# Optimization experiments

Measured on AMD Instinct MI355X. Metric: run time of the kernel, lower is better.

## Reference

```python
import jax, jax.numpy as jnp
import numpy as np

# DkNetCL (ConformalLayers): depth x [Conv2d(3x3, pad=1, no bias) + SRePro], then Linear(32768 -> 10).
# ConformalLayers algebraically fuses the cascade in conformal space; the equivalent Euclidean math
# per layer is: x <- conv(x); x <- x * 2*alpha^2 / (2*alpha^2 + ||x||^2), where ||x|| is the l2 norm
# of the ENTIRE flattened feature map of each sample (the sample is a single point in conformal space).
# alpha fixed to 1.0 (cl.SRePro() default is weight-adaptive; a constant keeps the reference deterministic).

DEPTH = 4
ALPHA = 1.0


def _conv(x, w):
    # x: [B, Cin, H, W], w: [Cout, Cin, 3, 3], stride 1, padding 1 (shape-preserving)
    return jax.lax.conv_general_dilated(
        x, w, window_strides=(1, 1), padding=((1, 1), (1, 1)),
        dimension_numbers=("NCHW", "OIHW", "NCHW"))


def _srepro(x, alpha):
    # per-sample squared norm over the whole feature map
    sq = jnp.sum(x * x, axis=(1, 2, 3), keepdims=True)  # [B,1,1,1]
    two_a2 = 2.0 * alpha * alpha
    return x * (two_a2 / (two_a2 + sq))


def setup_inputs() -> dict:
    key = jax.random.key(0)
    ks = jax.random.split(key, DEPTH + 2)
    B, H, W = 1024, 32, 32
    x = jax.random.normal(ks[0], (B, 3, H, W), jnp.float32)
    inp = {"x": x}
    cin = 3
    for i in range(DEPTH):
        fan_in = cin * 9
        inp[f"conv_w{i}"] = jax.random.normal(ks[1 + i], (32, cin, 3, 3), jnp.float32) / np.sqrt(fan_in).astype(np.float32)
        cin = 32
    flat = 32 * H * W  # 32768
    inp["fc_w"] = jax.random.normal(ks[-1], (10, flat), jnp.float32) / np.sqrt(flat).astype(np.float32)
    inp["fc_b"] = jnp.zeros((10,), jnp.float32)
    return inp


def reference(x, conv_w0, conv_w1, conv_w2, conv_w3, fc_w, fc_b):
    for w in (conv_w0, conv_w1, conv_w2, conv_w3):
        x = _srepro(_conv(x, w), ALPHA)
    x = x.reshape(x.shape[0], -1)  # [B, 32768]
    return x @ fc_w.T + fc_b  # [B, 10]
```

## Files before the change

### kernel.cpp

```cpp
#include <hip/hip_runtime.h>
#include <stdint.h>


typedef __bf16 bf16x8 __attribute__((ext_vector_type(8)));
typedef float f32x4 __attribute__((ext_vector_type(4)));
typedef unsigned short u16;
typedef unsigned int u32;

__device__ __forceinline__ u16 f2bf(float f) {
    union { float f; u32 i; } v; v.f = f;
    u32 r = v.i + 0x7FFFu + ((v.i >> 16) & 1u);
    return (u16)(r >> 16);
}
__device__ __forceinline__ float bf2f(u16 u) {
    union { u32 i; float f; } v; v.i = ((u32)u) << 16;
    return v.f;
}
union frag_cast { uint4 u; bf16x8 f; };

__global__ void prep_weights_k(const float* __restrict__ w0, const float* __restrict__ w1,
                               const float* __restrict__ w2, const float* __restrict__ w3,
                               u16* __restrict__ wfrag)
{
    int idx = blockIdx.x * 256 + threadIdx.x;
    if (idx >= 4 * 9 * 2 * 64) return;
    int lane  = idx & 63;
    int mh    = (idx >> 6) & 1;
    int tap   = (idx >> 7) % 9;
    int layer = (idx >> 7) / 9;
    const float* w = layer == 0 ? w0 : layer == 1 ? w1 : layer == 2 ? w2 : w3;
    int cin_act = (layer == 0) ? 3 : 32;
    int cout = mh * 16 + (lane & 15);
    int cin0 = (lane >> 4) * 8;
    int dy = tap / 3, dx = tap % 3;
    u16 v[8];
    for (int j = 0; j < 8; j++) {
        int cin = cin0 + j;
        float f = (cin < cin_act) ? w[((cout * cin_act + cin) * 3 + dy) * 3 + dx] : 0.f;
        v[j] = f2bf(f);
    }
    uint4 pack;
    pack.x = (u32)v[0] | ((u32)v[1] << 16);
    pack.y = (u32)v[2] | ((u32)v[3] << 16);
    pack.z = (u32)v[4] | ((u32)v[5] << 16);
    pack.w = (u32)v[6] | ((u32)v[7] << 16);
    reinterpret_cast<uint4*>(wfrag)[idx] = pack;
}

__global__ void prep_wfc_k(const float* __restrict__ fcw, u16* __restrict__ wfc)
{
    int idx = blockIdx.x * 256 + threadIdx.x;
    int lane = idx & 63, step = idx >> 6;
    int j = lane & 15, kq = lane >> 4;
    u16 hi[8], lo[8];
#pragma unroll
    for (int e = 0; e < 8; e++) {
        int k = step * 32 + kq * 8 + e;
        int c = k & 31, p = k >> 5;
        float f = (j < 10) ? fcw[j * 32768 + c * 1024 + p] : 0.f;
        u16 h = f2bf(f);
        hi[e] = h;
        lo[e] = f2bf(f - bf2f(h));
    }
    uint4 ph, pl;
    ph.x = (u32)hi[0] | ((u32)hi[1] << 16); ph.y = (u32)hi[2] | ((u32)hi[3] << 16);
    ph.z = (u32)hi[4] | ((u32)hi[5] << 16); ph.w = (u32)hi[6] | ((u32)hi[7] << 16);
    pl.x = (u32)lo[0] | ((u32)lo[1] << 16); pl.y = (u32)lo[2] | ((u32)lo[3] << 16);
    pl.z = (u32)lo[4] | ((u32)lo[5] << 16); pl.w = (u32)lo[6] | ((u32)lo[7] << 16);
    reinterpret_cast<uint4*>(wfc)[idx] = ph;
    reinterpret_cast<uint4*>(wfc)[65536 + idx] = pl;
}

__global__ void __launch_bounds__(256, 1)
net_k(const float* __restrict__ x, const u16* __restrict__ wfrag,
      u16* __restrict__ u4, float* __restrict__ c4)
{
    __shared__ u16 lds[2][32768];
    __shared__ float red[4][4];
    const int b = blockIdx.x;
    const int tid = threadIdx.x;
    const int lane = tid & 63;
    const int wv = tid >> 6;
    const int px = lane & 15;
    const int kq = lane >> 4;
    float vn[4] = {0.f, 0.f, 0.f, 0.f};

    const float* xb = x + (size_t)b * 3072;
#pragma unroll
    for (int it = 0; it < 16; it++) {
        int Q = it * 256 + tid;
        int pix = Q >> 2, q = Q & 3;
        uint4 val = make_uint4(0, 0, 0, 0);
        if (q == 0) {
            float f0 = xb[pix], f1 = xb[1024 + pix], f2 = xb[2048 + pix];
            val.x = (u32)f2bf(f0) | ((u32)f2bf(f1) << 16);
            val.y = (u32)f2bf(f2);
        }
        *reinterpret_cast<uint4*>(&lds[0][Q * 8]) = val;
    }

    const int orow0 = wv * 8;
#pragma unroll 1
    for (int l = 0; l < 4; l++) {
        bf16x8 W[3][3][2];
        const uint4* wl = reinterpret_cast<const uint4*>(wfrag + l * 9216);
#pragma unroll
        for (int dy = 0; dy < 3; dy++)
#pragma unroll
            for (int dx = 0; dx < 3; dx++)
#pragma unroll
                for (int mh = 0; mh < 2; mh++) {
                    frag_cast fc;
                    fc.u = wl[((dy * 3 + dx) * 2 + mh) * 64 + lane];
                    W[dy][dx][mh] = fc.f;
                }
        const u16* src = lds[l & 1];
        u16* dst = lds[(l & 1) ^ 1];
        __syncthreads();

#pragma unroll 1
        for (int ch = 0; ch < 4; ch++) {
            const int oA = orow0 + ch * 2;
            f32x4 accA[2][2]; f32x4 accB[2][2];
#pragma unroll
            for (int mh = 0; mh < 2; mh++)
#pragma unroll
                for (int nt = 0; nt < 2; nt++) { accA[mh][nt] = (f32x4)0.f; accB[mh][nt] = (f32x4)0.f; }

#pragma unroll
            for (int k = 0; k < 4; k++) {
                int ri = oA - 1 + k;
                if (ri >= 0 && ri < 32) {
                    bf16x8 bfr[2][3];
#pragma unroll
                    for (int nt = 0; nt < 2; nt++)
#pragma unroll
                        for (int d = 0; d < 3; d++) {
                            int xx = nt * 16 + px + d - 1;
                            bool oob = ((unsigned)xx >= 32u);
                            int xc = oob ? (nt * 16 + px) : xx;
                            frag_cast fc;
                            fc.u = *reinterpret_cast<const uint4*>(&src[(ri * 32 + xc) * 32 + kq * 8]);
                            if (oob) { fc.u.x = 0; fc.u.y = 0; fc.u.z = 0; fc.u.w = 0; }
                            bfr[nt][d] = fc.f;
                        }
                    if (k <= 2) {
#pragma unroll
                        for (int mh = 0; mh < 2; mh++)
#pragma unroll
                            for (int nt = 0; nt < 2; nt++)
#pragma unroll
                                for (int d = 0; d < 3; d++)
                                    accA[mh][nt] = __builtin_amdgcn_mfma_f32_16x16x32_bf16(
                                        W[k][d][mh], bfr[nt][d], accA[mh][nt], 0, 0, 0);
                    }
                    if (k >= 1) {
#pragma unroll
                        for (int mh = 0; mh < 2; mh++)
#pragma unroll
                            for (int nt = 0; nt < 2; nt++)
#pragma unroll
                                for (int d = 0; d < 3; d++)
                                    accB[mh][nt] = __builtin_amdgcn_mfma_f32_16x16x32_bf16(
                                        W[k - 1][d][mh], bfr[nt][d], accB[mh][nt], 0, 0, 0);
                    }
                }
            }
#pragma unroll
            for (int mh = 0; mh < 2; mh++)
#pragma unroll
                for (int nt = 0; nt < 2; nt++) {
                    f32x4 a = accA[mh][nt];
                    vn[l] += a[0]*a[0] + a[1]*a[1] + a[2]*a[2] + a[3]*a[3];
                    ushort4 h = make_ushort4(f2bf(a[0]), f2bf(a[1]), f2bf(a[2]), f2bf(a[3]));
                    *reinterpret_cast<ushort4*>(&dst[((oA * 32 + nt * 16 + px)) * 32 + mh * 16 + kq * 4]) = h;
                    f32x4 c = accB[mh][nt];
                    vn[l] += c[0]*c[0] + c[1]*c[1] + c[2]*c[2] + c[3]*c[3];
                    ushort4 h2 = make_ushort4(f2bf(c[0]), f2bf(c[1]), f2bf(c[2]), f2bf(c[3]));
                    *reinterpret_cast<ushort4*>(&dst[(((oA + 1) * 32 + nt * 16 + px)) * 32 + mh * 16 + kq * 4]) = h2;
                }
        }
    }

#pragma unroll
    for (int l = 0; l < 4; l++)
#pragma unroll
        for (int off = 32; off; off >>= 1) vn[l] += __shfl_xor(vn[l], off);
    if (lane == 0) {
#pragma unroll
        for (int l = 0; l < 4; l++) red[wv][l] = vn[l];
    }
    __syncthreads();
    float c = 1.f;
#pragma unroll
    for (int l = 0; l < 4; l++) {
        float n = red[0][l] + red[1][l] + red[2][l] + red[3][l];
        c = c * (2.f / (2.f + c * c * n));
    }
    if (tid == 0) c4[b] = c;

    u16* ub = u4 + (size_t)b * 32768;
#pragma unroll
    for (int it = 0; it < 16; it++) {
        int Q = it * 256 + tid;
        *reinterpret_cast<uint4*>(ub + Q * 8) =
            *reinterpret_cast<const uint4*>(&lds[0][Q * 8]);
    }
}

__global__ void __launch_bounds__(256)
fc_mfma_k(const u16* __restrict__ u4, const u16* __restrict__ wfc,
          float* __restrict__ tmp)
{
    const int lane = threadIdx.x & 63;
    const int wv = threadIdx.x >> 6;
    const int wid = blockIdx.x * 4 + wv;
    const int kc = wid & 31;
    const int st = wid >> 5;
    const int px = lane & 15, kq = lane >> 4;
    const uint4* Ah = reinterpret_cast<const uint4*>(wfc) + kc * 32 * 64 + lane;
    const uint4* Al = Ah + 65536;
    const u16* B = u4 + (size_t)(st * 16 + px) * 32768 + kc * 1024 + kq * 8;
    f32x4 acc = (f32x4)0.f;
#pragma unroll
    for (int s = 0; s < 32; s++) {
        frag_cast a, al, bb;
        a.u  = Ah[s * 64];
        al.u = Al[s * 64];
        bb.u = *reinterpret_cast<const uint4*>(B + s * 32);
        acc = __builtin_amdgcn_mfma_f32_16x16x32_bf16(a.f,  bb.f, acc, 0, 0, 0);
        acc = __builtin_amdgcn_mfma_f32_16x16x32_bf16(al.f, bb.f, acc, 0, 0, 0);
    }
    int sample = st * 16 + px;
#pragma unroll
    for (int r = 0; r < 4; r++) {
        int j = kq * 4 + r;
        if (j < 10) atomicAdd(&tmp[sample * 10 + j], acc[r]);
    }
}

__global__ void finalize_k(const float* __restrict__ tmp, const float* __restrict__ c4,
                           const float* __restrict__ fcb, float* __restrict__ out)
{
    int i = blockIdx.x * 256 + threadIdx.x;
    if (i >= 10240) return;
    int b = i / 10, j = i - b * 10;
    out[i] = c4[b] * tmp[i] + fcb[j];
}

extern "C" void kernel_launch(void* const* d_in, const int* in_sizes, int n_in,
                              void* d_out, int out_size, void* d_ws, size_t ws_size,
                              hipStream_t stream)
{
    const float* x   = (const float*)d_in[0];
    const float* cw0 = (const float*)d_in[1];
    const float* cw1 = (const float*)d_in[2];
    const float* cw2 = (const float*)d_in[3];
    const float* cw3 = (const float*)d_in[4];
    const float* fcw = (const float*)d_in[5];
    const float* fcb = (const float*)d_in[6];
    float* out = (float*)d_out;
    char* ws = (char*)d_ws;

    const size_t USZ = (size_t)1024 * 32768 * 2;
    u16* uA    = (u16*)ws;
    u16* wfrag = (u16*)(ws + USZ);
    u16* wfc   = (u16*)(ws + USZ + 81920);
    float* tmp = (float*)(ws + USZ + 81920 + 2097152);
    float* c4  = tmp + 10240;

    hipMemsetAsync(tmp, 0, 10240 * sizeof(float), stream);
    prep_weights_k<<<18, 256, 0, stream>>>(cw0, cw1, cw2, cw3, wfrag);
    prep_wfc_k<<<256, 256, 0, stream>>>(fcw, wfc);
    net_k<<<1024, 256, 0, stream>>>(x, wfrag, uA, c4);
    fc_mfma_k<<<512, 256, 0, stream>>>(uA, wfc, tmp);
    finalize_k<<<40, 256, 0, stream>>>(tmp, c4, fcb, out);
}
```

Baseline: 222.0 us.

## Double net_k block to 512 threads and XOR-swizzle LDS activation layout

Launches the fused conv kernel with 8 waves per block instead of 4, so each wave handles 4 output rows rather than 8. This raises latency hiding for a kernel that is otherwise limited to one block per CU by its 128 KB LDS. It also adds an XOR swizzle of the channel-chunk index inside the LDS activation layout to cut bank conflicts on the 16-byte fragment loads and 8-byte stores. The final copy-out is rewritten to unswizzle into the same global layout. The costs are more register pressure under the 512-thread launch bound and a longer block-level reduction.

```diff
diff --git a/kernel.cpp b/kernel.cpp
--- a/kernel.cpp
+++ b/kernel.cpp
@@ -17,6 +17,10 @@
     return v.f;
 }
 union frag_cast { uint4 u; bf16x8 f; };
+
+__device__ __forceinline__ int swz(int p, int c) {
+    return p * 32 + ((c ^ ((p >> 1) & 3)) * 8);
+}
 
 __global__ void prep_weights_k(const float* __restrict__ w0, const float* __restrict__ w1,
                                const float* __restrict__ w2, const float* __restrict__ w3,
@@ -71,12 +75,12 @@
     reinterpret_cast<uint4*>(wfc)[65536 + idx] = pl;
 }
 
-__global__ void __launch_bounds__(256, 1)
+__global__ void __launch_bounds__(512, 1)
 net_k(const float* __restrict__ x, const u16* __restrict__ wfrag,
       u16* __restrict__ u4, float* __restrict__ c4)
 {
     __shared__ u16 lds[2][32768];
-    __shared__ float red[4][4];
+    __shared__ float red[8][4];
     const int b = blockIdx.x;
     const int tid = threadIdx.x;
     const int lane = tid & 63;
@@ -87,19 +91,19 @@
 
     const float* xb = x + (size_t)b * 3072;
 #pragma unroll
-    for (int it = 0; it < 16; it++) {
-        int Q = it * 256 + tid;
-        int pix = Q >> 2, q = Q & 3;
+    for (int it = 0; it < 8; it++) {
+        int pix = it * 128 + wv * 16 + px;
+        int c = kq;
         uint4 val = make_uint4(0, 0, 0, 0);
-        if (q == 0) {
+        if (c == 0) {
             float f0 = xb[pix], f1 = xb[1024 + pix], f2 = xb[2048 + pix];
             val.x = (u32)f2bf(f0) | ((u32)f2bf(f1) << 16);
             val.y = (u32)f2bf(f2);
         }
-        *reinterpret_cast<uint4*>(&lds[0][Q * 8]) = val;
-    }
-
-    const int orow0 = wv * 8;
+        *reinterpret_cast<uint4*>(&lds[0][swz(pix, c)]) = val;
+    }
+
+    const int orow0 = wv * 4;
 #pragma unroll 1
     for (int l = 0; l < 4; l++) {
         bf16x8 W[3][3][2];
@@ -119,7 +123,7 @@
         __syncthreads();
 
 #pragma unroll 1
-        for (int ch = 0; ch < 4; ch++) {
+        for (int ch = 0; ch < 2; ch++) {
             const int oA = orow0 + ch * 2;
             f32x4 accA[2][2]; f32x4 accB[2][2];
 #pragma unroll
@@ -140,7 +144,7 @@
                             bool oob = ((unsigned)xx >= 32u);
                             int xc = oob ? (nt * 16 + px) : xx;
                             frag_cast fc;
-                            fc.u = *reinterpret_cast<const uint4*>(&src[(ri * 32 + xc) * 32 + kq * 8]);
+                            fc.u = *reinterpret_cast<const uint4*>(&src[swz(ri * 32 + xc, kq)]);
                             if (oob) { fc.u.x = 0; fc.u.y = 0; fc.u.z = 0; fc.u.w = 0; }
                             bfr[nt][d] = fc.f;
                         }
@@ -170,14 +174,18 @@
             for (int mh = 0; mh < 2; mh++)
 #pragma unroll
                 for (int nt = 0; nt < 2; nt++) {
+                    int cch = mh * 2 + (kq >> 1);
+                    int sub = (kq & 1) * 4;
                     f32x4 a = accA[mh][nt];
                     vn[l] += a[0]*a[0] + a[1]*a[1] + a[2]*a[2] + a[3]*a[3];
                     ushort4 h = make_ushort4(f2bf(a[0]), f2bf(a[1]), f2bf(a[2]), f2bf(a[3]));
-                    *reinterpret_cast<ushort4*>(&dst[((oA * 32 + nt * 16 + px)) * 32 + mh * 16 + kq * 4]) = h;
+                    int P0 = oA * 32 + nt * 16 + px;
+                    *reinterpret_cast<ushort4*>(&dst[swz(P0, cch) + sub]) = h;
                     f32x4 c = accB[mh][nt];
                     vn[l] += c[0]*c[0] + c[1]*c[1] + c[2]*c[2] + c[3]*c[3];
                     ushort4 h2 = make_ushort4(f2bf(c[0]), f2bf(c[1]), f2bf(c[2]), f2bf(c[3]));
-                    *reinterpret_cast<ushort4*>(&dst[(((oA + 1) * 32 + nt * 16 + px)) * 32 + mh * 16 + kq * 4]) = h2;
+                    int P1 = (oA + 1) * 32 + nt * 16 + px;
+                    *reinterpret_cast<ushort4*>(&dst[swz(P1, cch) + sub]) = h2;
                 }
         }
     }
@@ -194,17 +202,20 @@
     float c = 1.f;
 #pragma unroll
     for (int l = 0; l < 4; l++) {
-        float n = red[0][l] + red[1][l] + red[2][l] + red[3][l];
+        float n = 0.f;
+#pragma unroll
+        for (int w = 0; w < 8; w++) n += red[w][l];
         c = c * (2.f / (2.f + c * c * n));
     }
     if (tid == 0) c4[b] = c;
 
     u16* ub = u4 + (size_t)b * 32768;
 #pragma unroll
-    for (int it = 0; it < 16; it++) {
-        int Q = it * 256 + tid;
-        *reinterpret_cast<uint4*>(ub + Q * 8) =
-            *reinterpret_cast<const uint4*>(&lds[0][Q * 8]);
+    for (int it = 0; it < 8; it++) {
+        int pix = it * 128 + wv * 16 + px;
+        int cch = kq;
+        *reinterpret_cast<uint4*>(ub + pix * 32 + cch * 8) =
+            *reinterpret_cast<const uint4*>(&lds[0][swz(pix, cch)]);
     }
 }
 
@@ -272,7 +283,7 @@
     hipMemsetAsync(tmp, 0, 10240 * sizeof(float), stream);
     prep_weights_k<<<18, 256, 0, stream>>>(cw0, cw1, cw2, cw3, wfrag);
     prep_wfc_k<<<256, 256, 0, stream>>>(fcw, wfc);
-    net_k<<<1024, 256, 0, stream>>>(x, wfrag, uA, c4);
+    net_k<<<1024, 512, 0, stream>>>(x, wfrag, uA, c4);
     fc_mfma_k<<<512, 256, 0, stream>>>(uA, wfc, tmp);
     finalize_k<<<40, 256, 0, stream>>>(tmp, c4, fcb, out);
 }
```

New measurement: 193.3 us. 1.15x faster.
